# Kernel optimization log

Hardware: AMD Instinct MI355X
Metric: run time of the kernel (lower is better)

## Reference

```python
import jax, jax.numpy as jnp
import numpy as np

N_NODES = 100000
N_EDGES = 1600000
IN_DIM = 64
HID = 64
EDGE_DIM = 1
NUM_GRAPHS = 1000
SCALE = 0.05


def setup_inputs() -> dict:
    key = jax.random.key(0)
    ks = jax.random.split(key, 20)
    x = jax.random.normal(ks[0], (N_NODES, IN_DIM), dtype=jnp.float32)
    edge_index = jax.random.randint(ks[1], (2, N_EDGES), 0, N_NODES, dtype=jnp.int64)
    edge_attr = jax.random.normal(ks[2], (N_EDGES, EDGE_DIM), dtype=jnp.float32)
    batch = jnp.sort(jax.random.randint(ks[3], (N_NODES,), 0, NUM_GRAPHS, dtype=jnp.int64))
    p = lambda k, shp: SCALE * jax.random.normal(k, shp, dtype=jnp.float32)
    return {
        "x": x, "edge_index": edge_index, "edge_attr": edge_attr, "batch": batch,
        # conv1 MLP + edge lin
        "W1a": p(ks[4], (IN_DIM, HID)), "b1a": p(ks[5], (HID,)),
        "W1b": p(ks[6], (HID, HID)), "b1b": p(ks[7], (HID,)),
        "We1": p(ks[8], (EDGE_DIM, IN_DIM)), "be1": p(ks[9], (IN_DIM,)),
        # conv2 MLP + edge lin
        "W2a": p(ks[10], (HID, HID)), "b2a": p(ks[11], (HID,)),
        "W2b": p(ks[12], (HID, HID)), "b2b": p(ks[13], (HID,)),
        "We2": p(ks[14], (EDGE_DIM, HID)), "be2": p(ks[15], (HID,)),
        # classifier
        "Wc1": p(ks[16], (HID, HID)), "bc1": p(ks[17], (HID,)),
        "Wc2": p(ks[18], (HID, 1)), "bc2": p(ks[19], (1,)),
    }


def _gine(x, src, dst, e_proj, Wa, ba, Wb, bb):
    # message: ReLU(x_src + projected edge feature); scatter-sum to target
    msg = jax.nn.relu(x[src] + e_proj)                      # [E, D]
    agg = jax.ops.segment_sum(msg, dst, num_segments=x.shape[0])
    h = x + agg                                             # eps = 0 (default)
    return jax.nn.relu(h @ Wa + ba) @ Wb + bb               # GIN MLP


def reference(x, edge_index, edge_attr, batch,
              W1a, b1a, W1b, b1b, We1, be1,
              W2a, b2a, W2b, b2b, We2, be2,
              Wc1, bc1, Wc2, bc2):
    src, dst = edge_index[0], edge_index[1]
    h = _gine(x, src, dst, edge_attr @ We1 + be1, W1a, b1a, W1b, b1b)
    h = jax.nn.relu(h)  # dropout is identity in eval mode
    h = _gine(h, src, dst, edge_attr @ We2 + be2, W2a, b2a, W2b, b2b)
    h = jax.nn.relu(h)
    # global mean pool over graphs
    sums = jax.ops.segment_sum(h, batch, num_segments=NUM_GRAPHS)
    cnts = jax.ops.segment_sum(jnp.ones((h.shape[0], 1), h.dtype), batch, num_segments=NUM_GRAPHS)
    pooled = sums / jnp.maximum(cnts, 1.0)                  # [G, HID]
    return jax.nn.relu(pooled @ Wc1 + bc1) @ Wc2 + bc2      # [G, 1]
```

## Files before the change

kernel.cpp:

```cpp
#include <hip/hip_runtime.h>

#define N_NODES    100000
#define N_EDGES    1600000
#define DIM        64
#define NUM_GRAPHS 1000
#define CONV_BLK   3125
#define PAD        72

#define SLICES     512
#define SLICE_E    3125
#define NBUCK      782
#define CAP4       3072

typedef __attribute__((ext_vector_type(8))) short bf16x8;
typedef __attribute__((ext_vector_type(4))) float f32x4;

__device__ __forceinline__ unsigned short f2bf(float f) {
    unsigned int b = __float_as_uint(f);
    b += 0x7FFFu + ((b >> 16) & 1u);
    return (unsigned short)(b >> 16);
}

__device__ __forceinline__ float4 ntload_f4(const float* p) {
    f32x4 v = __builtin_nontemporal_load((const f32x4*)p);
    return make_float4(v.x, v.y, v.z, v.w);
}

__global__ __launch_bounds__(256) void prep(
    const int* __restrict__ ei, const float* __restrict__ x,
    int* __restrict__ hist, int* __restrict__ bucketTotal,
    unsigned short* __restrict__ x16)
{
    __shared__ int lh[NBUCK];
    int blk = blockIdx.x, t = threadIdx.x;
    if (blk < SLICES) {
        for (int i = t; i < NBUCK; i += 256) lh[i] = 0;
        __syncthreads();
        const int* dsts = ei + N_EDGES + blk * SLICE_E;
        for (int k = t; k < SLICE_E; k += 256)
            atomicAdd(&lh[dsts[k] >> 7], 1);
        __syncthreads();
        for (int i = t; i < NBUCK; i += 256) {
            int h = lh[i];
            hist[blk * NBUCK + i] = h;
            if (h) atomicAdd(&bucketTotal[i], h);
        }
    } else {
        int tt = (blk - SLICES) * 256 + t;
        if (tt < N_NODES * DIM / 8) {
            int base = tt * 8;
            float4 f0 = ntload_f4(x + base);
            float4 f1 = ntload_f4(x + base + 4);
            uint4 o;
            o.x = (unsigned)f2bf(f0.x) | ((unsigned)f2bf(f0.y) << 16);
            o.y = (unsigned)f2bf(f0.z) | ((unsigned)f2bf(f0.w) << 16);
            o.z = (unsigned)f2bf(f1.x) | ((unsigned)f2bf(f1.y) << 16);
            o.w = (unsigned)f2bf(f1.z) | ((unsigned)f2bf(f1.w) << 16);
            *(uint4*)(x16 + base) = o;
        }
    }
}

__global__ __launch_bounds__(1024) void csr_c2a(
    const int* __restrict__ bucketTotal, int* __restrict__ bucketStart)
{
    __shared__ int sc[1024];
    int t = threadIdx.x;
    int v = (t < NBUCK) ? bucketTotal[t] : 0;
    sc[t] = v;
    __syncthreads();
    for (int o = 1; o < 1024; o <<= 1) {
        int u = (t >= o) ? sc[t - o] : 0;
        __syncthreads();
        sc[t] += u;
        __syncthreads();
    }
    if (t < NBUCK) bucketStart[t] = sc[t] - v;
    if (t == NBUCK - 1) bucketStart[NBUCK] = sc[t];
}

__global__ __launch_bounds__(512) void csr_c2b(
    const int* __restrict__ hist, const int* __restrict__ bucketStart,
    int* __restrict__ off)
{
    __shared__ int sc[512];
    int b = blockIdx.x, t = threadIdx.x;
    int v = hist[t * NBUCK + b];
    sc[t] = v;
    __syncthreads();
    for (int o = 1; o < 512; o <<= 1) {
        int u = (t >= o) ? sc[t - o] : 0;
        __syncthreads();
        sc[t] += u;
        __syncthreads();
    }
    off[b * SLICES + t] = bucketStart[b] + sc[t] - v;
}

__global__ __launch_bounds__(256) void csr_c3(
    const int* __restrict__ ei, const float* __restrict__ ea,
    const int* __restrict__ hist, const int* __restrict__ off,
    int2* __restrict__ tmp)
{
    __shared__ int2 staging[SLICE_E];
    __shared__ int  lstart[NBUCK + 1];
    __shared__ int  garr[NBUCK];
    __shared__ int  lcur[NBUCK];
    __shared__ unsigned short barr[SLICE_E];
    __shared__ int  part[256];

    int s = blockIdx.x, t = threadIdx.x;

    int h[4];
    int mysum = 0;
    #pragma unroll
    for (int j = 0; j < 4; ++j) {
        int b = 4 * t + j;
        h[j] = (b < NBUCK) ? hist[s * NBUCK + b] : 0;
        mysum += h[j];
    }
    part[t] = mysum;
    for (int i = t; i < NBUCK; i += 256) {
        garr[i] = off[i * SLICES + s];
        lcur[i] = 0;
    }
    __syncthreads();
    for (int o = 1; o < 256; o <<= 1) {
        int u = (t >= o) ? part[t - o] : 0;
        __syncthreads();
        part[t] += u;
        __syncthreads();
    }
    int run = part[t] - mysum;
    #pragma unroll
    for (int j = 0; j < 4; ++j) {
        int b = 4 * t + j;
        if (b < NBUCK) lstart[b] = run;
        run += h[j];
    }
    if (t == 0) lstart[NBUCK] = SLICE_E;
    __syncthreads();

    #pragma unroll
    for (int j = 0; j < 4; ++j) {
        int b = 4 * t + j;
        if (b < NBUCK)
            for (int i = lstart[b]; i < lstart[b + 1]; ++i)
                barr[i] = (unsigned short)b;
    }
    __syncthreads();

    for (int k = t; k < SLICE_E; k += 256) {
        int e   = s * SLICE_E + k;
        int src = ei[e];
        int dst = ei[N_EDGES + e];
        float a = ea[e];
        int b   = dst >> 7;
        int p   = lstart[b] + atomicAdd(&lcur[b], 1);
        staging[p] = make_int2(((dst & 127) << 17) | src, __float_as_int(a));
    }
    __syncthreads();

    for (int i = t; i < SLICE_E; i += 256) {
        int b = barr[i];
        tmp[garr[b] + (i - lstart[b])] = staging[i];
    }
}

__global__ __launch_bounds__(256) void csr_c4(
    const int2* __restrict__ tmp, const int* __restrict__ bucketStart,
    int2* __restrict__ csr_e, int* __restrict__ rowptr)
{
    __shared__ int2 staging[CAP4];
    __shared__ int  nh[128];
    __shared__ int  nscan[128];
    __shared__ int  ncur[128];

    int b = blockIdx.x, t = threadIdx.x;
    int lo = bucketStart[b], hi = bucketStart[b + 1];
    int cnt = hi - lo;
    int node0 = b << 7;
    int nn = min(128, N_NODES - node0);

    if (t < 128) { nh[t] = 0; ncur[t] = 0; }
    __syncthreads();

    int2 r[12];
    int nr = 0;
    for (int k = t; k < cnt; k += 256) {
        int2 v = tmp[lo + k];
        r[nr++] = v;
        atomicAdd(&nh[v.x >> 17], 1);
    }
    __syncthreads();

    if (t < 128) nscan[t] = nh[t];
    __syncthreads();
    for (int o = 1; o < 128; o <<= 1) {
        int u = (t >= o && t < 128) ? nscan[t - o] : 0;
        __syncthreads();
        if (t < 128) nscan[t] += u;
        __syncthreads();
    }
    if (t < 128) nscan[t] -= nh[t];
    __syncthreads();

    if (t < nn) rowptr[node0 + t] = lo + nscan[t];
    if (b == NBUCK - 1 && t == 0) rowptr[N_NODES] = N_EDGES;

    for (int k = 0; k < nr; ++k) {
        int dl = r[k].x >> 17;
        int p  = nscan[dl] + atomicAdd(&ncur[dl], 1);
        staging[p] = r[k];
    }
    __syncthreads();

    for (int i = t; i < cnt; i += 256) {
        int2 v = staging[i];
        csr_e[lo + i] = make_int2((v.x & 0x1FFFF) << 4, v.y);
    }
}

template<bool SELF32>
__global__ __launch_bounds__(512, 8) void gine_mfma(
    const uint2* __restrict__ g2,
    const float* __restrict__ self32,
    const int*   __restrict__ rowptr,
    const int2*  __restrict__ csr_e,
    const float* __restrict__ We, const float* __restrict__ be,
    const float* __restrict__ Wa, const float* __restrict__ ba,
    const float* __restrict__ Wb, const float* __restrict__ bb,
    unsigned int* __restrict__ out16)
{
    __shared__ short sWat[64 * PAD];
    __shared__ short sWbt[64 * PAD];
    __shared__ short h16[32 * PAD];
    __shared__ short t16[32 * PAD];

    int t = threadIdx.x;
    for (int i = t; i < 4096; i += 512) {
        int k = i >> 6, n = i & 63;
        sWat[n * PAD + k] = (short)f2bf(Wa[i]);
        sWbt[n * PAD + k] = (short)f2bf(Wb[i]);
    }
    int wave = t >> 6;
    int lane = t & 63;
    int quad = lane >> 4;
    int l15  = lane & 15;
    int slot = wave * 4 + quad;
    int d0   = l15 * 4;
    float4 wp = *(const float4*)(We + d0);
    float4 bp = *(const float4*)(be + d0);
    int mtile = wave & 1;
    int ntile = wave >> 1;
    int col   = ntile * 16 + l15;
    int am    = mtile * 16 + l15;
    float bav = ba[col], bbv = bb[col];
    __syncthreads();

    for (int base = blockIdx.x * 32; base < N_NODES; base += gridDim.x * 32) {
        int  node  = base + slot;
        bool valid = node < N_NODES;
        int beg = 0, deg = 0;
        if (valid) { beg = rowptr[node]; deg = rowptr[node + 1] - beg; }
        int dm = deg;
        dm = max(dm, __shfl_xor(dm, 16));
        dm = max(dm, __shfl_xor(dm, 32));

        float4 agg = make_float4(0.f, 0.f, 0.f, 0.f);
        #define EDGE4(rr, uu, cond)                                              \
        {                                                                        \
            float s = (cond) ? 1.f : 0.f, av = __int_as_float(rr.y);             \
            float e0 = __uint_as_float(uu.x << 16);                              \
            float e1 = __uint_as_float(uu.x & 0xFFFF0000u);                      \
            float e2 = __uint_as_float(uu.y << 16);                              \
            float e3 = __uint_as_float(uu.y & 0xFFFF0000u);                      \
            agg.x = fmaf(s, fmaxf(e0 + fmaf(av, wp.x, bp.x), 0.f), agg.x);       \
            agg.y = fmaf(s, fmaxf(e1 + fmaf(av, wp.y, bp.y), 0.f), agg.y);       \
            agg.z = fmaf(s, fmaxf(e2 + fmaf(av, wp.z, bp.z), 0.f), agg.z);       \
            agg.w = fmaf(s, fmaxf(e3 + fmaf(av, wp.w, bp.w), 0.f), agg.w);       \
        }
        for (int j = 0; j < dm; j += 4) {
            int2 r0 = csr_e[beg + ((j + 0) < deg ? j + 0 : 0)];
            int2 r1 = csr_e[beg + ((j + 1) < deg ? j + 1 : 0)];
            int2 r2 = csr_e[beg + ((j + 2) < deg ? j + 2 : 0)];
            int2 r3 = csr_e[beg + ((j + 3) < deg ? j + 3 : 0)];
            uint2 u0 = g2[r0.x + l15];
            uint2 u1 = g2[r1.x + l15];
            uint2 u2 = g2[r2.x + l15];
            uint2 u3 = g2[r3.x + l15];
            EDGE4(r0, u0, (j + 0) < deg)
            EDGE4(r1, u1, (j + 1) < deg)
            EDGE4(r2, u2, (j + 2) < deg)
            EDGE4(r3, u3, (j + 3) < deg)
        }
        #undef EDGE4
        if (valid) {
            if (SELF32) {
                float4 sv = *(const float4*)(self32 + (size_t)node * DIM + d0);
                agg.x += sv.x; agg.y += sv.y; agg.z += sv.z; agg.w += sv.w;
            } else {
                uint2 u = g2[node * 16 + l15];
                agg.x += __uint_as_float(u.x << 16);
                agg.y += __uint_as_float(u.x & 0xFFFF0000u);
                agg.z += __uint_as_float(u.y << 16);
                agg.w += __uint_as_float(u.y & 0xFFFF0000u);
            }
        }
        {
            unsigned lo = (unsigned)f2bf(agg.x) | ((unsigned)f2bf(agg.y) << 16);
            unsigned hi = (unsigned)f2bf(agg.z) | ((unsigned)f2bf(agg.w) << 16);
            *(uint2*)&h16[slot * PAD + d0] = make_uint2(lo, hi);
        }
        __syncthreads();

        f32x4 acc = {bav, bav, bav, bav};
        #pragma unroll
        for (int s = 0; s < 2; ++s) {
            bf16x8 a = *(const bf16x8*)&h16[am * PAD + s * 32 + quad * 8];
            bf16x8 b = *(const bf16x8*)&sWat[col * PAD + s * 32 + quad * 8];
            acc = __builtin_amdgcn_mfma_f32_16x16x32_bf16(a, b, acc, 0, 0, 0);
        }
        #pragma unroll
        for (int r = 0; r < 4; ++r) {
            int row = mtile * 16 + quad * 4 + r;
            t16[row * PAD + col] = (short)f2bf(fmaxf(acc[r], 0.f));
        }
        __syncthreads();

        f32x4 acc2 = {bbv, bbv, bbv, bbv};
        #pragma unroll
        for (int s = 0; s < 2; ++s) {
            bf16x8 a = *(const bf16x8*)&t16[am * PAD + s * 32 + quad * 8];
            bf16x8 b = *(const bf16x8*)&sWbt[col * PAD + s * 32 + quad * 8];
            acc2 = __builtin_amdgcn_mfma_f32_16x16x32_bf16(a, b, acc2, 0, 0, 0);
        }
        #pragma unroll
        for (int r = 0; r < 4; ++r) {
            int row = mtile * 16 + quad * 4 + r;
            h16[row * PAD + col] = (short)f2bf(fmaxf(acc2[r], 0.f));
        }
        __syncthreads();
        {
            int nn = t >> 4, dd = (t & 15) * 2;
            if (base + nn < N_NODES) {
                uint2 v = *(const uint2*)&h16[nn * PAD + dd * 2];
                *(uint2*)&out16[(size_t)(base + nn) * 32 + dd] = v;
            }
        }
        __syncthreads();
    }
}

__device__ __forceinline__ int lbound(const int* __restrict__ a, int key) {
    int lo = 0, hi = N_NODES;
    while (lo < hi) {
        int mid = (lo + hi) >> 1;
        if (a[mid] < key) lo = mid + 1; else hi = mid;
    }
    return lo;
}

__global__ __launch_bounds__(256) void pool_cls(
    const unsigned int* __restrict__ B16b,
    const int* __restrict__ batch,
    const float* __restrict__ Wc1,  const float* __restrict__ bc1,
    const float* __restrict__ Wc2,  const float* __restrict__ bc2,
    float* __restrict__ out)
{
    __shared__ float sW[64 * 64];
    __shared__ float sp[4][64];

    int t = threadIdx.x;
    for (int i = t; i < 64 * 64; i += 256) sW[i] = Wc1[i];

    int nl   = t >> 6;
    int lane = t & 63;
    int g    = blockIdx.x * 4 + nl;

    int p = lane & 31, h = lane >> 5;
    if (g < NUM_GRAPHS) {
        int s = lbound(batch, g);
        int e = lbound(batch, g + 1);
        float2 sum = make_float2(0.f, 0.f);
        for (int i = s + h; i < e; i += 2) {
            unsigned u = B16b[(size_t)i * 32 + p];
            sum.x += __uint_as_float(u << 16);
            sum.y += __uint_as_float(u & 0xFFFF0000u);
        }
        sum.x += __shfl_xor(sum.x, 32);
        sum.y += __shfl_xor(sum.y, 32);
        if (h == 0) {
            float inv = 1.f / (float)max(e - s, 1);
            sp[nl][2 * p]     = sum.x * inv;
            sp[nl][2 * p + 1] = sum.y * inv;
        }
    } else if (h == 0) {
        sp[nl][2 * p] = 0.f;
        sp[nl][2 * p + 1] = 0.f;
    }
    __syncthreads();

    float acc = bc1[lane];
    #pragma unroll
    for (int k = 0; k < 64; ++k)
        acc = fmaf(sp[nl][k], sW[k * 64 + lane], acc);
    float tv = fmaxf(acc, 0.f) * Wc2[lane];

    #pragma unroll
    for (int off = 32; off > 0; off >>= 1)
        tv += __shfl_down(tv, off);

    if (lane == 0 && g < NUM_GRAPHS) out[g] = tv + bc2[0];
}

extern "C" void kernel_launch(void* const* d_in, const int* in_sizes, int n_in,
                              void* d_out, int out_size, void* d_ws, size_t ws_size,
                              hipStream_t stream) {
    const float* x     = (const float*)d_in[0];
    const int*   ei    = (const int*)  d_in[1];
    const float* ea    = (const float*)d_in[2];
    const int*   batch = (const int*)  d_in[3];
    const float* W1a = (const float*)d_in[4];
    const float* b1a = (const float*)d_in[5];
    const float* W1b = (const float*)d_in[6];
    const float* b1b = (const float*)d_in[7];
    const float* We1 = (const float*)d_in[8];
    const float* be1 = (const float*)d_in[9];
    const float* W2a = (const float*)d_in[10];
    const float* b2a = (const float*)d_in[11];
    const float* W2b = (const float*)d_in[12];
    const float* b2b = (const float*)d_in[13];
    const float* We2 = (const float*)d_in[14];
    const float* be2 = (const float*)d_in[15];
    const float* Wc1 = (const float*)d_in[16];
    const float* bc1 = (const float*)d_in[17];
    const float* Wc2 = (const float*)d_in[18];
    const float* bc2 = (const float*)d_in[19];

    int2*           csr_e  = (int2*)d_ws;
    unsigned short* x16    = (unsigned short*)(csr_e + N_EDGES);
    unsigned short* B16    = x16 + (size_t)N_NODES * DIM;
    unsigned short* B16b   = B16 + (size_t)N_NODES * DIM;
    int2*           tmp    = (int2*)B16b;
    int*            hist   = (int*)(B16b + (size_t)N_NODES * DIM);
    int*            off    = hist + SLICES * NBUCK;
    int*            bucketTotal = off + NBUCK * SLICES;
    int*            bucketStart = bucketTotal + NBUCK;
    int*            rowptr = bucketStart + (NBUCK + 1);

    hipMemsetAsync(bucketTotal, 0, NBUCK * sizeof(int), stream);

    prep<<<SLICES + CONV_BLK, 256, 0, stream>>>(ei, x, hist, bucketTotal, x16);
    csr_c2a<<<1, 1024, 0, stream>>>(bucketTotal, bucketStart);
    csr_c2b<<<NBUCK, 512, 0, stream>>>(hist, bucketStart, off);
    csr_c3<<<SLICES, 256, 0, stream>>>(ei, ea, hist, off, tmp);
    csr_c4<<<NBUCK, 256, 0, stream>>>(tmp, bucketStart, csr_e, rowptr);

    gine_mfma<true><<<1024, 512, 0, stream>>>(
        (const uint2*)x16, x, rowptr, csr_e,
        We1, be1, W1a, b1a, W1b, b1b, (unsigned int*)B16);

    gine_mfma<false><<<1024, 512, 0, stream>>>(
        (const uint2*)B16, nullptr, rowptr, csr_e,
        We2, be2, W2a, b2a, W2b, b2b, (unsigned int*)B16b);

    pool_cls<<<(NUM_GRAPHS + 3) / 4, 256, 0, stream>>>(
        (const unsigned int*)B16b, batch, Wc1, bc1, Wc2, bc2, (float*)d_out);
}
```

Baseline: 302.3 us.

## Balance edge aggregation per 32-node tile with LDS atomic segment flushes

Replaces the one-node-per-16-lane-group aggregation, whose loop length is bounded by the maximum degree in the wavefront, with an edge-balanced scheme. Each tile's contiguous CSR edge range is split evenly across 32 lane groups. Partial sums are flushed into an fp32 shared buffer via LDS atomics whenever the destination slot changes. The destination slot is packed into the high bits of the CSR source word to make this possible, at the cost of extra LDS space, atomics, an extra barrier, and loss of the 4-way load unrolling.

Measured after the change: 384.4 us. 1.27x slower.

```diff
diff --git a/kernel.cpp b/kernel.cpp
--- a/kernel.cpp
+++ b/kernel.cpp
@@ -6,6 +6,8 @@
 #define NUM_GRAPHS 1000
 #define CONV_BLK   3125
 #define PAD        72
+#define H32S       65
+#define NTILE      3125
 
 #define SLICES     512
 #define SLICE_E    3125
@@ -217,7 +219,9 @@
 
     for (int i = t; i < cnt; i += 256) {
         int2 v = staging[i];
-        csr_e[lo + i] = make_int2((v.x & 0x1FFFF) << 4, v.y);
+        int src  = v.x & 0x1FFFF;
+        int slot = (v.x >> 17) & 31;
+        csr_e[lo + i] = make_int2((slot << 25) | (src << 4), v.y);
     }
 }
 
@@ -234,6 +238,7 @@
 {
     __shared__ short sWat[64 * PAD];
     __shared__ short sWbt[64 * PAD];
+    __shared__ float h32[32 * H32S];
     __shared__ short h16[32 * PAD];
     __shared__ short t16[32 * PAD];
 
@@ -247,7 +252,7 @@
     int lane = t & 63;
     int quad = lane >> 4;
     int l15  = lane & 15;
-    int slot = wave * 4 + quad;
+    int qg   = t >> 4;
     int d0   = l15 * 4;
     float4 wp = *(const float4*)(We + d0);
     float4 bp = *(const float4*)(be + d0);
@@ -258,73 +263,87 @@
     float bav = ba[col], bbv = bb[col];
     __syncthreads();
 
-    for (int base = blockIdx.x * 32; base < N_NODES; base += gridDim.x * 32) {
-        int  node  = base + slot;
-        bool valid = node < N_NODES;
-        int beg = 0, deg = 0;
-        if (valid) { beg = rowptr[node]; deg = rowptr[node + 1] - beg; }
-        int dm = deg;
-        dm = max(dm, __shfl_xor(dm, 16));
-        dm = max(dm, __shfl_xor(dm, 32));
-
-        float4 agg = make_float4(0.f, 0.f, 0.f, 0.f);
-        #define EDGE4(rr, uu, cond)                                              \
-        {                                                                        \
-            float s = (cond) ? 1.f : 0.f, av = __int_as_float(rr.y);             \
-            float e0 = __uint_as_float(uu.x << 16);                              \
-            float e1 = __uint_as_float(uu.x & 0xFFFF0000u);                      \
-            float e2 = __uint_as_float(uu.y << 16);                              \
-            float e3 = __uint_as_float(uu.y & 0xFFFF0000u);                      \
-            agg.x = fmaf(s, fmaxf(e0 + fmaf(av, wp.x, bp.x), 0.f), agg.x);       \
-            agg.y = fmaf(s, fmaxf(e1 + fmaf(av, wp.y, bp.y), 0.f), agg.y);       \
-            agg.z = fmaf(s, fmaxf(e2 + fmaf(av, wp.z, bp.z), 0.f), agg.z);       \
-            agg.w = fmaf(s, fmaxf(e3 + fmaf(av, wp.w, bp.w), 0.f), agg.w);       \
-        }
-        for (int j = 0; j < dm; j += 4) {
-            int2 r0 = csr_e[beg + ((j + 0) < deg ? j + 0 : 0)];
-            int2 r1 = csr_e[beg + ((j + 1) < deg ? j + 1 : 0)];
-            int2 r2 = csr_e[beg + ((j + 2) < deg ? j + 2 : 0)];
-            int2 r3 = csr_e[beg + ((j + 3) < deg ? j + 3 : 0)];
-            uint2 u0 = g2[r0.x + l15];
-            uint2 u1 = g2[r1.x + l15];
-            uint2 u2 = g2[r2.x + l15];
-            uint2 u3 = g2[r3.x + l15];
-            EDGE4(r0, u0, (j + 0) < deg)
-            EDGE4(r1, u1, (j + 1) < deg)
-            EDGE4(r2, u2, (j + 2) < deg)
-            EDGE4(r3, u3, (j + 3) < deg)
-        }
-        #undef EDGE4
-        if (valid) {
+    for (int tile = blockIdx.x; tile < NTILE; tile += gridDim.x) {
+        int base = tile * 32;
+
+        {
+            int slot = qg;
             if (SELF32) {
-                float4 sv = *(const float4*)(self32 + (size_t)node * DIM + d0);
-                agg.x += sv.x; agg.y += sv.y; agg.z += sv.z; agg.w += sv.w;
+                float4 sv = *(const float4*)(self32 + (size_t)(base + slot) * DIM + d0);
+                *(float4*)&h32[slot * H32S + d0] = sv;
             } else {
-                uint2 u = g2[node * 16 + l15];
-                agg.x += __uint_as_float(u.x << 16);
-                agg.y += __uint_as_float(u.x & 0xFFFF0000u);
-                agg.z += __uint_as_float(u.y << 16);
-                agg.w += __uint_as_float(u.y & 0xFFFF0000u);
+                uint2 u = g2[(size_t)(base + slot) * 16 + l15];
+                float4 sv;
+                sv.x = __uint_as_float(u.x << 16);
+                sv.y = __uint_as_float(u.x & 0xFFFF0000u);
+                sv.z = __uint_as_float(u.y << 16);
+                sv.w = __uint_as_float(u.y & 0xFFFF0000u);
+                *(float4*)&h32[slot * H32S + d0] = sv;
             }
         }
+        __syncthreads();
+
+        int e0 = rowptr[base];
+        int e1 = rowptr[base + 32];
+        int cnt = e1 - e0;
+        int L  = (cnt + 31) >> 5;
+        int cs = e0 + qg * L;
+        int ce = min(cs + L, e1);
+
+        float4 acc = make_float4(0.f, 0.f, 0.f, 0.f);
+        int cur = -1;
+        if (cs < ce) {
+            int2 r = csr_e[cs];
+            for (int e = cs; e < ce; ++e) {
+                int2 rn = (e + 1 < ce) ? csr_e[e + 1] : r;
+                uint2 u = g2[(r.x & 0x1FFFF0) + l15];
+                int slot = ((unsigned)r.x) >> 25;
+                if (slot != cur) {
+                    if (cur >= 0) {
+                        float* p = &h32[cur * H32S + d0];
+                        atomicAdd(p + 0, acc.x);
+                        atomicAdd(p + 1, acc.y);
+                        atomicAdd(p + 2, acc.z);
+                        atomicAdd(p + 3, acc.w);
+                    }
+                    cur = slot;
+                    acc = make_float4(0.f, 0.f, 0.f, 0.f);
+                }
+                float av = __int_as_float(r.y);
+                acc.x += fmaxf(__uint_as_float(u.x << 16)         + fmaf(av, wp.x, bp.x), 0.f);
+                acc.y += fmaxf(__uint_as_float(u.x & 0xFFFF0000u) + fmaf(av, wp.y, bp.y), 0.f);
+                acc.z += fmaxf(__uint_as_float(u.y << 16)         + fmaf(av, wp.z, bp.z), 0.f);
+                acc.w += fmaxf(__uint_as_float(u.y & 0xFFFF0000u) + fmaf(av, wp.w, bp.w), 0.f);
+                r = rn;
+            }
+            float* p = &h32[cur * H32S + d0];
+            atomicAdd(p + 0, acc.x);
+            atomicAdd(p + 1, acc.y);
+            atomicAdd(p + 2, acc.z);
+            atomicAdd(p + 3, acc.w);
+        }
+        __syncthreads();
+
         {
-            unsigned lo = (unsigned)f2bf(agg.x) | ((unsigned)f2bf(agg.y) << 16);
-            unsigned hi = (unsigned)f2bf(agg.z) | ((unsigned)f2bf(agg.w) << 16);
+            int slot = qg;
+            float4 v = *(const float4*)&h32[slot * H32S + d0];
+            unsigned lo = (unsigned)f2bf(v.x) | ((unsigned)f2bf(v.y) << 16);
+            unsigned hi = (unsigned)f2bf(v.z) | ((unsigned)f2bf(v.w) << 16);
             *(uint2*)&h16[slot * PAD + d0] = make_uint2(lo, hi);
         }
         __syncthreads();
 
-        f32x4 acc = {bav, bav, bav, bav};
+        f32x4 acc1 = {bav, bav, bav, bav};
         #pragma unroll
         for (int s = 0; s < 2; ++s) {
             bf16x8 a = *(const bf16x8*)&h16[am * PAD + s * 32 + quad * 8];
             bf16x8 b = *(const bf16x8*)&sWat[col * PAD + s * 32 + quad * 8];
-            acc = __builtin_amdgcn_mfma_f32_16x16x32_bf16(a, b, acc, 0, 0, 0);
+            acc1 = __builtin_amdgcn_mfma_f32_16x16x32_bf16(a, b, acc1, 0, 0, 0);
         }
         #pragma unroll
         for (int r = 0; r < 4; ++r) {
             int row = mtile * 16 + quad * 4 + r;
-            t16[row * PAD + col] = (short)f2bf(fmaxf(acc[r], 0.f));
+            t16[row * PAD + col] = (short)f2bf(fmaxf(acc1[r], 0.f));
         }
         __syncthreads();
 
@@ -343,10 +362,8 @@
         __syncthreads();
         {
             int nn = t >> 4, dd = (t & 15) * 2;
-            if (base + nn < N_NODES) {
-                uint2 v = *(const uint2*)&h16[nn * PAD + dd * 2];
-                *(uint2*)&out16[(size_t)(base + nn) * 32 + dd] = v;
-            }
+            uint2 v = *(const uint2*)&h16[nn * PAD + dd * 2];
+            *(uint2*)&out16[(size_t)(base + nn) * 32 + dd] = v;
         }
         __syncthreads();
     }
```

## Sort tile nodes by degree for wave balance and merge CSR scan kernels

Applied to the files above, without the earlier changes.

Inside each 32-node tile of the GINE kernel, nodes are ranked by in-degree and assigned to slots so that the 16-lane groups within a wave process nodes of similar degree. This cuts idle lanes in the max-degree loop. The two bucket-scan kernels are fused into one, each block recomputing its bucket start by reduction, which saves a launch. The first layer also reads the self feature from bf16 instead of fp32. Together these add a few extra barriers per tile and slightly lower first-layer precision.

After: 306.7 us. No clear change (+1.5%).

```diff
diff --git a/kernel.cpp b/kernel.cpp
--- a/kernel.cpp
+++ b/kernel.cpp
@@ -6,6 +6,7 @@
 #define NUM_GRAPHS 1000
 #define CONV_BLK   3125
 #define PAD        72
+#define NTILE      3125
 
 #define SLICES     512
 #define SLICE_E    3125
@@ -61,40 +62,34 @@
     }
 }
 
-__global__ __launch_bounds__(1024) void csr_c2a(
-    const int* __restrict__ bucketTotal, int* __restrict__ bucketStart)
-{
-    __shared__ int sc[1024];
-    int t = threadIdx.x;
-    int v = (t < NBUCK) ? bucketTotal[t] : 0;
-    sc[t] = v;
-    __syncthreads();
-    for (int o = 1; o < 1024; o <<= 1) {
-        int u = (t >= o) ? sc[t - o] : 0;
-        __syncthreads();
-        sc[t] += u;
-        __syncthreads();
-    }
-    if (t < NBUCK) bucketStart[t] = sc[t] - v;
-    if (t == NBUCK - 1) bucketStart[NBUCK] = sc[t];
-}
-
-__global__ __launch_bounds__(512) void csr_c2b(
-    const int* __restrict__ hist, const int* __restrict__ bucketStart,
-    int* __restrict__ off)
-{
+__global__ __launch_bounds__(512) void csr_c2(
+    const int* __restrict__ hist, const int* __restrict__ bucketTotal,
+    int* __restrict__ bucketStart, int* __restrict__ off)
+{
+    __shared__ int red[512];
     __shared__ int sc[512];
     int b = blockIdx.x, t = threadIdx.x;
+
+    int part = 0;
+    for (int i = t; i < b; i += 512) part += bucketTotal[i];
+    red[t] = part;
     int v = hist[t * NBUCK + b];
     sc[t] = v;
     __syncthreads();
+    for (int o = 256; o > 0; o >>= 1) {
+        if (t < o) red[t] += red[t + o];
+        __syncthreads();
+    }
+    int bstart = red[0];
     for (int o = 1; o < 512; o <<= 1) {
         int u = (t >= o) ? sc[t - o] : 0;
         __syncthreads();
         sc[t] += u;
         __syncthreads();
     }
-    off[b * SLICES + t] = bucketStart[b] + sc[t] - v;
+    off[b * SLICES + t] = bstart + sc[t] - v;
+    if (t == 0) bucketStart[b] = bstart;
+    if (b == NBUCK - 1 && t == 511) bucketStart[NBUCK] = bstart + sc[t];
 }
 
 __global__ __launch_bounds__(256) void csr_c3(
@@ -221,10 +216,8 @@
     }
 }
 
-template<bool SELF32>
 __global__ __launch_bounds__(512, 8) void gine_mfma(
     const uint2* __restrict__ g2,
-    const float* __restrict__ self32,
     const int*   __restrict__ rowptr,
     const int2*  __restrict__ csr_e,
     const float* __restrict__ We, const float* __restrict__ be,
@@ -236,6 +229,9 @@
     __shared__ short sWbt[64 * PAD];
     __shared__ short h16[32 * PAD];
     __shared__ short t16[32 * PAD];
+    __shared__ int   srp[33];
+    __shared__ int   sdeg[32];
+    __shared__ unsigned char sperm[32];
 
     int t = threadIdx.x;
     for (int i = t; i < 4096; i += 512) {
@@ -258,11 +254,28 @@
     float bav = ba[col], bbv = bb[col];
     __syncthreads();
 
-    for (int base = blockIdx.x * 32; base < N_NODES; base += gridDim.x * 32) {
-        int  node  = base + slot;
-        bool valid = node < N_NODES;
-        int beg = 0, deg = 0;
-        if (valid) { beg = rowptr[node]; deg = rowptr[node + 1] - beg; }
+    for (int tile = blockIdx.x; tile < NTILE; tile += gridDim.x) {
+        int base = tile * 32;
+
+        if (t < 33) srp[t] = rowptr[base + t];
+        __syncthreads();
+        if (t < 32) sdeg[t] = srp[t + 1] - srp[t];
+        __syncthreads();
+        if (t < 32) {
+            int di = sdeg[t];
+            int rank = 0;
+            #pragma unroll
+            for (int j = 0; j < 32; ++j) {
+                int dj = sdeg[j];
+                rank += (dj > di) || (dj == di && j < t);
+            }
+            sperm[rank] = (unsigned char)t;
+        }
+        __syncthreads();
+
+        int pn  = sperm[slot];
+        int beg = srp[pn];
+        int deg = sdeg[pn];
         int dm = deg;
         dm = max(dm, __shfl_xor(dm, 16));
         dm = max(dm, __shfl_xor(dm, 32));
@@ -295,22 +308,17 @@
             EDGE4(r3, u3, (j + 3) < deg)
         }
         #undef EDGE4
-        if (valid) {
-            if (SELF32) {
-                float4 sv = *(const float4*)(self32 + (size_t)node * DIM + d0);
-                agg.x += sv.x; agg.y += sv.y; agg.z += sv.z; agg.w += sv.w;
-            } else {
-                uint2 u = g2[node * 16 + l15];
-                agg.x += __uint_as_float(u.x << 16);
-                agg.y += __uint_as_float(u.x & 0xFFFF0000u);
-                agg.z += __uint_as_float(u.y << 16);
-                agg.w += __uint_as_float(u.y & 0xFFFF0000u);
-            }
+        {
+            uint2 u = g2[(size_t)(base + pn) * 16 + l15];
+            agg.x += __uint_as_float(u.x << 16);
+            agg.y += __uint_as_float(u.x & 0xFFFF0000u);
+            agg.z += __uint_as_float(u.y << 16);
+            agg.w += __uint_as_float(u.y & 0xFFFF0000u);
         }
         {
             unsigned lo = (unsigned)f2bf(agg.x) | ((unsigned)f2bf(agg.y) << 16);
             unsigned hi = (unsigned)f2bf(agg.z) | ((unsigned)f2bf(agg.w) << 16);
-            *(uint2*)&h16[slot * PAD + d0] = make_uint2(lo, hi);
+            *(uint2*)&h16[pn * PAD + d0] = make_uint2(lo, hi);
         }
         __syncthreads();
 
@@ -343,10 +351,8 @@
         __syncthreads();
         {
             int nn = t >> 4, dd = (t & 15) * 2;
-            if (base + nn < N_NODES) {
-                uint2 v = *(const uint2*)&h16[nn * PAD + dd * 2];
-                *(uint2*)&out16[(size_t)(base + nn) * 32 + dd] = v;
-            }
+            uint2 v = *(const uint2*)&h16[nn * PAD + dd * 2];
+            *(uint2*)&out16[(size_t)(base + nn) * 32 + dd] = v;
         }
         __syncthreads();
     }
@@ -452,17 +458,16 @@
     hipMemsetAsync(bucketTotal, 0, NBUCK * sizeof(int), stream);
 
     prep<<<SLICES + CONV_BLK, 256, 0, stream>>>(ei, x, hist, bucketTotal, x16);
-    csr_c2a<<<1, 1024, 0, stream>>>(bucketTotal, bucketStart);
-    csr_c2b<<<NBUCK, 512, 0, stream>>>(hist, bucketStart, off);
+    csr_c2<<<NBUCK, 512, 0, stream>>>(hist, bucketTotal, bucketStart, off);
     csr_c3<<<SLICES, 256, 0, stream>>>(ei, ea, hist, off, tmp);
     csr_c4<<<NBUCK, 256, 0, stream>>>(tmp, bucketStart, csr_e, rowptr);
 
-    gine_mfma<true><<<1024, 512, 0, stream>>>(
-        (const uint2*)x16, x, rowptr, csr_e,
+    gine_mfma<<<1024, 512, 0, stream>>>(
+        (const uint2*)x16, rowptr, csr_e,
         We1, be1, W1a, b1a, W1b, b1b, (unsigned int*)B16);
 
-    gine_mfma<false><<<1024, 512, 0, stream>>>(
-        (const uint2*)B16, nullptr, rowptr, csr_e,
+    gine_mfma<<<1024, 512, 0, stream>>>(
+        (const uint2*)B16, rowptr, csr_e,
         We2, be2, W2a, b2a, W2b, b2b, (unsigned int*)B16b);
 
     pool_cls<<<(NUM_GRAPHS + 3) / 4, 256, 0, stream>>>(
```
